# Kernel tuning notes

Measured on AMD Instinct MI355X. Metric: run time of the kernel, lower is better.

The kernel has to match this reference:

```python
import jax, jax.numpy as jnp
import numpy as np
import math

H = 8          # num_heads
HD = 64        # head_dim = hidden_dim // num_heads
LN_EPS = 1e-5


def setup_inputs() -> dict:
    key = jax.random.key(0)
    ks = jax.random.split(key, 16)
    B, N, L, D = 16, 1024, 7, 512
    s = 1.0 / math.sqrt(D)
    current_features = jax.random.normal(ks[0], (B, N, D), jnp.float32)
    lagged_features = jax.random.normal(ks[1], (B, N, L, D), jnp.float32)
    lag_weights = jnp.ones((L,), jnp.float32)
    Wq = jax.random.normal(ks[2], (D, D), jnp.float32) * s
    bq = jnp.zeros((D,), jnp.float32)
    Wk = jax.random.normal(ks[3], (D, D), jnp.float32) * s
    bk = jnp.zeros((D,), jnp.float32)
    Wv = jax.random.normal(ks[4], (D, D), jnp.float32) * s
    bv = jnp.zeros((D,), jnp.float32)
    Wo = jax.random.normal(ks[5], (D, D), jnp.float32) * s
    bo = jnp.zeros((D,), jnp.float32)
    adj = jax.random.uniform(ks[6], (N, N), jnp.float32)
    adj_prior = adj / (jnp.sum(adj, axis=-1, keepdims=True) + 1e-8)
    ln_g = jnp.ones((D,), jnp.float32)
    ln_b = jnp.zeros((D,), jnp.float32)
    return dict(current_features=current_features, lagged_features=lagged_features,
                lag_weights=lag_weights, Wq=Wq, bq=bq, Wk=Wk, bk=bk, Wv=Wv, bv=bv,
                Wo=Wo, bo=bo, adj_prior=adj_prior, ln_g=ln_g, ln_b=ln_b)


def _layer_norm(x, g, b):
    mu = jnp.mean(x, axis=-1, keepdims=True)
    var = jnp.mean(jnp.square(x - mu), axis=-1, keepdims=True)
    return (x - mu) * jax.lax.rsqrt(var + LN_EPS) * g + b


def reference(current_features, lagged_features, lag_weights, Wq, bq, Wk, bk,
              Wv, bv, Wo, bo, adj_prior, ln_g, ln_b):
    B, N, D = current_features.shape
    # lag-weighted aggregation of past states
    lag_w = jax.nn.softmax(lag_weights)
    lagged_agg = jnp.einsum('bnld,l->bnd', lagged_features, lag_w)
    # projections (torch Linear: x @ W.T + b)
    Q = current_features @ Wq.T + bq
    K = lagged_agg @ Wk.T + bk
    V = lagged_agg @ Wv.T + bv
    Q = Q.reshape(B, N, H, HD)
    K = K.reshape(B, N, H, HD)
    V = V.reshape(B, N, H, HD)
    scale = math.sqrt(HD)
    # scores [B, H, N, N] with additive adjacency bias
    scores = jnp.einsum('bnhd,bmhd->bhnm', Q, K) / scale
    scores = scores + adj_prior[None, None, :, :] * 0.5
    attn = jax.nn.softmax(scores, axis=-1)
    out = jnp.einsum('bhnm,bmhd->bnhd', attn, V).reshape(B, N, D)
    out = out @ Wo.T + bo
    return _layer_norm(current_features + out, ln_g, ln_b)
```

## Files before the change

### kernel.cpp

```cpp
#include <hip/hip_runtime.h>
#include <math.h>

#define B_  16
#define N_  1024
#define L_  7
#define D_  512
#define H_  8
#define HD_ 64
#define BN_ (B_ * N_)

typedef __attribute__((ext_vector_type(4))) float f32x4;
typedef __attribute__((ext_vector_type(8))) short bf16x8;

__device__ __forceinline__ unsigned short f2bf(float f) {
  unsigned int u = __float_as_uint(f);
  u += 0x7fffu + ((u >> 16) & 1u);
  return (unsigned short)(u >> 16);
}
__device__ __forceinline__ unsigned int pack2(float lo, float hi) {
  return (unsigned int)f2bf(lo) | ((unsigned int)f2bf(hi) << 16);
}
__device__ __forceinline__ void load_lds16(const unsigned short* g, unsigned short* s) {
  __builtin_amdgcn_global_load_lds(
      (const __attribute__((address_space(1))) void*)g,
      (__attribute__((address_space(3))) void*)s, 16, 0, 0);
}

__global__ __launch_bounds__(256)
void cast_bf16_kernel(const float* __restrict__ src, unsigned short* __restrict__ dst,
                      int n8) {
  const int i = blockIdx.x * 256 + threadIdx.x;
  if (i >= n8) return;
  const float4 a = ((const float4*)src)[2 * i];
  const float4 b = ((const float4*)src)[2 * i + 1];
  uint4 o;
  o.x = pack2(a.x, a.y); o.y = pack2(a.z, a.w);
  o.z = pack2(b.x, b.y); o.w = pack2(b.z, b.w);
  ((uint4*)dst)[i] = o;
}

__global__ __launch_bounds__(256)
void lag_agg_bf16_kernel(const float* __restrict__ lf, const float* __restrict__ lw,
                         unsigned short* __restrict__ out) {
  const int i = blockIdx.x * 256 + threadIdx.x;
  float wv[L_];
  float m = -INFINITY;
#pragma unroll
  for (int l = 0; l < L_; ++l) { wv[l] = lw[l]; m = fmaxf(m, wv[l]); }
  float s = 0.f;
#pragma unroll
  for (int l = 0; l < L_; ++l) { wv[l] = __expf(wv[l] - m); s += wv[l]; }
  const float inv = 1.f / s;

  const int d8 = i & (D_ / 8 - 1);
  const int bn = i >> 6;
  const float* src = lf + (size_t)bn * (L_ * D_) + d8 * 8;
  float acc[8] = {};
#pragma unroll
  for (int l = 0; l < L_; ++l) {
    const float4 v0 = *(const float4*)(src + l * D_);
    const float4 v1 = *(const float4*)(src + l * D_ + 4);
    const float wl = wv[l] * inv;
    acc[0] += v0.x * wl; acc[1] += v0.y * wl; acc[2] += v0.z * wl; acc[3] += v0.w * wl;
    acc[4] += v1.x * wl; acc[5] += v1.y * wl; acc[6] += v1.z * wl; acc[7] += v1.w * wl;
  }
  uint4 o;
  o.x = pack2(acc[0], acc[1]); o.y = pack2(acc[2], acc[3]);
  o.z = pack2(acc[4], acc[5]); o.w = pack2(acc[6], acc[7]);
  ((uint4*)out)[i] = o;
}

template<int MODE>
__global__ __launch_bounds__(256)
void gemm_bf16_kernel(const unsigned short* __restrict__ A,
                      const unsigned short* __restrict__ W,
                      const float* __restrict__ bias,
                      void* __restrict__ Cout) {
  __shared__ unsigned short As[128 * 64];
  __shared__ unsigned short Bs[128 * 64];
  const int t = threadIdx.x;
  const int w = t >> 6, l = t & 63;
  const int wm = w >> 1, wn = w & 1;
  const int lc = l & 15, lg = l >> 4;
  const int m0 = blockIdx.y << 7, n0 = blockIdx.x << 7;
  const int srow = l >> 3, sc = l & 7;

  f32x4 acc[4][4];
#pragma unroll
  for (int i = 0; i < 4; ++i)
#pragma unroll
    for (int j = 0; j < 4; ++j)
#pragma unroll
      for (int e = 0; e < 4; ++e) acc[i][j][e] = 0.f;

  for (int k0 = 0; k0 < D_; k0 += 64) {
    __syncthreads();
#pragma unroll
    for (int i = 0; i < 4; ++i) {
      const int rb = (w << 5) + (i << 3);
      const int row = rb + srow;
      const int c = sc ^ (row & 7);
      load_lds16(A + (size_t)(m0 + row) * D_ + k0 + (c << 3), As + rb * 64);
      load_lds16(W + (size_t)(n0 + row) * D_ + k0 + (c << 3), Bs + rb * 64);
    }
    __syncthreads();
#pragma unroll
    for (int kb = 0; kb < 2; ++kb) {
      bf16x8 af[4], bfr[4];
#pragma unroll
      for (int mi = 0; mi < 4; ++mi) {
        const int row = (wm << 6) + (mi << 4) + lc;
        const int pos = ((kb << 2) + lg) ^ (row & 7);
        af[mi] = *(const bf16x8*)(As + row * 64 + (pos << 3));
      }
#pragma unroll
      for (int ni = 0; ni < 4; ++ni) {
        const int row = (wn << 6) + (ni << 4) + lc;
        const int pos = ((kb << 2) + lg) ^ (row & 7);
        bfr[ni] = *(const bf16x8*)(Bs + row * 64 + (pos << 3));
      }
#pragma unroll
      for (int mi = 0; mi < 4; ++mi)
#pragma unroll
        for (int ni = 0; ni < 4; ++ni)
          acc[mi][ni] = __builtin_amdgcn_mfma_f32_16x16x32_bf16(
              af[mi], bfr[ni], acc[mi][ni], 0, 0, 0);
    }
  }
#pragma unroll
  for (int ni = 0; ni < 4; ++ni) {
    const int n = n0 + (wn << 6) + (ni << 4) + lc;
    const float bv = bias[n];
#pragma unroll
    for (int mi = 0; mi < 4; ++mi) {
      const int mb = m0 + (wm << 6) + (mi << 4) + (lg << 2);
      if (MODE == 2) {
        float* O = (float*)Cout;
#pragma unroll
        for (int e = 0; e < 4; ++e)
          O[(size_t)(mb + e) * D_ + n] = acc[mi][ni][e] + bv;
      } else if (MODE == 0) {
        unsigned short* O = (unsigned short*)Cout;
#pragma unroll
        for (int e = 0; e < 4; ++e)
          O[(size_t)(mb + e) * D_ + n] = f2bf(acc[mi][ni][e] + bv);
      } else {
        unsigned short* O = (unsigned short*)Cout;
        const int bb = mb >> 10, hh = n >> 6, d = n & 63;
        uint2 pk;
        pk.x = pack2(acc[mi][ni][0] + bv, acc[mi][ni][1] + bv);
        pk.y = pack2(acc[mi][ni][2] + bv, acc[mi][ni][3] + bv);
        *(uint2*)(O + ((size_t)((bb << 3) + hh) * HD_ + d) * N_ + (mb & 1023)) = pk;
      }
    }
  }
}

__global__ __launch_bounds__(256)
void attn_bf16_kernel(const unsigned short* __restrict__ Q,
                      const unsigned short* __restrict__ K,
                      const unsigned short* __restrict__ Vt,
                      const float* __restrict__ adj,
                      unsigned short* __restrict__ Out) {
  const int bh = blockIdx.y, b = bh >> 3, h = bh & 7;
  const int q0 = blockIdx.x << 6;
  const int t = threadIdx.x, w = t >> 6, l = t & 63;
  const int lc = l & 15, lg = l >> 4;
  __shared__ unsigned short Qs[64 * 64];
  __shared__ unsigned short Ks[64 * 64];
  __shared__ unsigned short Vs[64 * 64];
  const unsigned short* Qg = Q + (size_t)b * N_ * D_ + h * HD_;
  const unsigned short* Kg = K + (size_t)b * N_ * D_ + h * HD_;
  const unsigned short* Vg = Vt + (size_t)((b << 3) + h) * HD_ * N_;

#pragma unroll
  for (int i = 0; i < 2; ++i) {
    const int rb = (w << 4) + (i << 3);
    const int row = rb + (l >> 3);
    const int c = (l & 7) ^ (row & 7);
    load_lds16(Qg + (size_t)(q0 + row) * D_ + (c << 3), Qs + rb * 64);
  }

  float m_r = -INFINITY, l_r = 0.f;
  f32x4 o[4];
#pragma unroll
  for (int di = 0; di < 4; ++di)
#pragma unroll
    for (int e = 0; e < 4; ++e) o[di][e] = 0.f;
  const int myq = q0 + (w << 4) + lc;

  for (int kt = 0; kt < 16; ++kt) {
    const int kv0 = kt << 6;
#pragma unroll
    for (int i = 0; i < 2; ++i) {
      const int rb = (w << 4) + (i << 3);
      const int row = rb + (l >> 3);
      const int c = (l & 7) ^ (row & 7);
      load_lds16(Kg + (size_t)(kv0 + row) * D_ + (c << 3), Ks + rb * 64);
      load_lds16(Vg + (size_t)row * N_ + kv0 + (c << 3), Vs + rb * 64);
    }
    f32x4 aj[4];
#pragma unroll
    for (int ni = 0; ni < 4; ++ni)
      aj[ni] = *(const f32x4*)(adj + (size_t)myq * N_ + kv0 + (ni << 4) + (lg << 2));
    __syncthreads();

    bf16x8 qf[2];
#pragma unroll
    for (int kb = 0; kb < 2; ++kb) {
      const int row = (w << 4) + lc;
      const int pos = ((kb << 2) + lg) ^ (row & 7);
      qf[kb] = *(const bf16x8*)(Qs + row * 64 + (pos << 3));
    }
    f32x4 st[4];
#pragma unroll
    for (int ni = 0; ni < 4; ++ni)
#pragma unroll
      for (int e = 0; e < 4; ++e) st[ni][e] = 0.f;
#pragma unroll
    for (int ni = 0; ni < 4; ++ni)
#pragma unroll
      for (int kb = 0; kb < 2; ++kb) {
        const int row = (ni << 4) + lc;
        const int pos = ((kb << 2) + lg) ^ (row & 7);
        const bf16x8 kf = *(const bf16x8*)(Ks + row * 64 + (pos << 3));
        st[ni] = __builtin_amdgcn_mfma_f32_16x16x32_bf16(kf, qf[kb], st[ni], 0, 0, 0);
      }

    float tmax = -INFINITY;
#pragma unroll
    for (int ni = 0; ni < 4; ++ni)
#pragma unroll
      for (int e = 0; e < 4; ++e) {
        const float v = st[ni][e] * 0.125f + 0.5f * aj[ni][e];
        st[ni][e] = v;
        tmax = fmaxf(tmax, v);
      }
    tmax = fmaxf(tmax, __shfl_xor(tmax, 16));
    tmax = fmaxf(tmax, __shfl_xor(tmax, 32));
    const float mnew = fmaxf(m_r, tmax);
    const float alpha = __expf(m_r - mnew);
    float ts = 0.f;
#pragma unroll
    for (int ni = 0; ni < 4; ++ni)
#pragma unroll
      for (int e = 0; e < 4; ++e) {
        const float p = __expf(st[ni][e] - mnew);
        st[ni][e] = p;
        ts += p;
      }
    ts += __shfl_xor(ts, 16);
    ts += __shfl_xor(ts, 32);
    l_r = l_r * alpha + ts;
    m_r = mnew;
#pragma unroll
    for (int di = 0; di < 4; ++di)
#pragma unroll
      for (int e = 0; e < 4; ++e) o[di][e] *= alpha;

    unsigned int p2[4][2];
#pragma unroll
    for (int ni = 0; ni < 4; ++ni) {
      p2[ni][0] = pack2(st[ni][0], st[ni][1]);
      p2[ni][1] = pack2(st[ni][2], st[ni][3]);
    }
    const int sA = lc + ((lg & 1) << 5);
    const int sB = sA + 16;
    const bool hiq = lg >= 2;
#pragma unroll
    for (int kb = 0; kb < 2; ++kb) {
      const unsigned int dA0 = (unsigned int)__shfl((int)p2[2 * kb][0], sA);
      const unsigned int dA1 = (unsigned int)__shfl((int)p2[2 * kb][1], sA);
      const unsigned int dA2 = (unsigned int)__shfl((int)p2[2 * kb][0], sB);
      const unsigned int dA3 = (unsigned int)__shfl((int)p2[2 * kb][1], sB);
      const unsigned int dB0 = (unsigned int)__shfl((int)p2[2 * kb + 1][0], sA);
      const unsigned int dB1 = (unsigned int)__shfl((int)p2[2 * kb + 1][1], sA);
      const unsigned int dB2 = (unsigned int)__shfl((int)p2[2 * kb + 1][0], sB);
      const unsigned int dB3 = (unsigned int)__shfl((int)p2[2 * kb + 1][1], sB);
      union { unsigned int u[4]; bf16x8 v; } pb;
      pb.u[0] = hiq ? dB0 : dA0;
      pb.u[1] = hiq ? dB1 : dA1;
      pb.u[2] = hiq ? dB2 : dA2;
      pb.u[3] = hiq ? dB3 : dA3;
#pragma unroll
      for (int di = 0; di < 4; ++di) {
        const int row = (di << 4) + lc;
        const int pos = ((kb << 2) + lg) ^ (row & 7);
        const bf16x8 vf = *(const bf16x8*)(Vs + row * 64 + (pos << 3));
        o[di] = __builtin_amdgcn_mfma_f32_16x16x32_bf16(vf, pb.v, o[di], 0, 0, 0);
      }
    }
    __syncthreads();
  }
  const float inv = 1.f / l_r;
  unsigned short* Ob = Out + (size_t)(b * N_ + q0 + (w << 4) + lc) * D_ + h * HD_;
#pragma unroll
  for (int di = 0; di < 4; ++di) {
    uint2 pk;
    pk.x = pack2(o[di][0] * inv, o[di][1] * inv);
    pk.y = pack2(o[di][2] * inv, o[di][3] * inv);
    *(uint2*)(Ob + (di << 4) + (lg << 2)) = pk;
  }
}

__global__ __launch_bounds__(256)
void ln_kernel(float* __restrict__ Y, const float* __restrict__ Xr,
               const float* __restrict__ g, const float* __restrict__ bta) {
  const int row  = (blockIdx.x << 2) + (threadIdx.x >> 6);
  const int lane = threadIdx.x & 63;
  float* yrow = Y + (size_t)row * D_;
  const float* xrow = Xr + (size_t)row * D_;
  const int c0 = lane << 3;

  const float4 y0 = *(const float4*)(yrow + c0);
  const float4 y1 = *(const float4*)(yrow + c0 + 4);
  const float4 r0 = *(const float4*)(xrow + c0);
  const float4 r1 = *(const float4*)(xrow + c0 + 4);
  float x[8] = {y0.x + r0.x, y0.y + r0.y, y0.z + r0.z, y0.w + r0.w,
                y1.x + r1.x, y1.y + r1.y, y1.z + r1.z, y1.w + r1.w};

  float sum = 0.f;
#pragma unroll
  for (int u = 0; u < 8; ++u) sum += x[u];
#pragma unroll
  for (int off = 32; off >= 1; off >>= 1) sum += __shfl_xor(sum, off);
  const float mu = sum * (1.f / D_);

  float vs = 0.f;
#pragma unroll
  for (int u = 0; u < 8; ++u) { const float d = x[u] - mu; vs += d * d; }
#pragma unroll
  for (int off = 32; off >= 1; off >>= 1) vs += __shfl_xor(vs, off);
  const float var = vs * (1.f / D_) + 1e-5f;
  float rinv = rsqrtf(var);
  rinv = rinv * (1.5f - 0.5f * var * rinv * rinv);

  const float4 g0 = *(const float4*)(g + c0);
  const float4 g1 = *(const float4*)(g + c0 + 4);
  const float4 b0 = *(const float4*)(bta + c0);
  const float4 b1 = *(const float4*)(bta + c0 + 4);
  float4 o0, o1;
  o0.x = (x[0] - mu) * rinv * g0.x + b0.x;
  o0.y = (x[1] - mu) * rinv * g0.y + b0.y;
  o0.z = (x[2] - mu) * rinv * g0.z + b0.z;
  o0.w = (x[3] - mu) * rinv * g0.w + b0.w;
  o1.x = (x[4] - mu) * rinv * g1.x + b1.x;
  o1.y = (x[5] - mu) * rinv * g1.y + b1.y;
  o1.z = (x[6] - mu) * rinv * g1.z + b1.z;
  o1.w = (x[7] - mu) * rinv * g1.w + b1.w;
  *(float4*)(yrow + c0) = o0;
  *(float4*)(yrow + c0 + 4) = o1;
}

extern "C" void kernel_launch(void* const* d_in, const int* in_sizes, int n_in,
                              void* d_out, int out_size, void* d_ws, size_t ws_size,
                              hipStream_t stream) {
  const float* cur = (const float*)d_in[0];
  const float* lf  = (const float*)d_in[1];
  const float* lw  = (const float*)d_in[2];
  const float* Wq  = (const float*)d_in[3];
  const float* bq  = (const float*)d_in[4];
  const float* Wk  = (const float*)d_in[5];
  const float* bk  = (const float*)d_in[6];
  const float* Wv  = (const float*)d_in[7];
  const float* bv  = (const float*)d_in[8];
  const float* Wo  = (const float*)d_in[9];
  const float* bo  = (const float*)d_in[10];
  const float* adj = (const float*)d_in[11];
  const float* lng = (const float*)d_in[12];
  const float* lnb = (const float*)d_in[13];
  float* out = (float*)d_out;

  const size_t NE = (size_t)BN_ * D_;
  unsigned short* wsb   = (unsigned short*)d_ws;
  unsigned short* curb  = wsb;
  unsigned short* laggb = wsb + NE;
  unsigned short* Qb    = wsb + 2 * NE;
  unsigned short* Kb    = wsb + 3 * NE;
  unsigned short* Vtb   = wsb + 4 * NE;
  unsigned short* attnb = wsb + 5 * NE;
  unsigned short* Wqb   = wsb + 6 * NE;
  unsigned short* Wkb   = Wqb + (size_t)D_ * D_;
  unsigned short* Wvb   = Wkb + (size_t)D_ * D_;
  unsigned short* Wob   = Wvb + (size_t)D_ * D_;

  cast_bf16_kernel<<<BN_ * D_ / 8 / 256, 256, 0, stream>>>(cur, curb, BN_ * D_ / 8);
  cast_bf16_kernel<<<D_ * D_ / 8 / 256, 256, 0, stream>>>(Wq, Wqb, D_ * D_ / 8);
  cast_bf16_kernel<<<D_ * D_ / 8 / 256, 256, 0, stream>>>(Wk, Wkb, D_ * D_ / 8);
  cast_bf16_kernel<<<D_ * D_ / 8 / 256, 256, 0, stream>>>(Wv, Wvb, D_ * D_ / 8);
  cast_bf16_kernel<<<D_ * D_ / 8 / 256, 256, 0, stream>>>(Wo, Wob, D_ * D_ / 8);
  lag_agg_bf16_kernel<<<BN_ * D_ / 8 / 256, 256, 0, stream>>>(lf, lw, laggb);

  const dim3 gg(D_ / 128, BN_ / 128);
  gemm_bf16_kernel<0><<<gg, 256, 0, stream>>>(curb,  Wqb, bq, (void*)Qb);
  gemm_bf16_kernel<0><<<gg, 256, 0, stream>>>(laggb, Wkb, bk, (void*)Kb);
  gemm_bf16_kernel<1><<<gg, 256, 0, stream>>>(laggb, Wvb, bv, (void*)Vtb);
  attn_bf16_kernel<<<dim3(N_ / 64, B_ * H_), 256, 0, stream>>>(Qb, Kb, Vtb, adj, attnb);
  gemm_bf16_kernel<2><<<gg, 256, 0, stream>>>(attnb, Wob, bo, (void*)out);
  ln_kernel<<<BN_ / 4, 256, 0, stream>>>(out, cur, lng, lnb);
}
```

Measured before the change: 573.4 us.

## Double-buffer GEMM and attention tiles, batch QKV GEMMs and weight casts

The GEMM and attention kernels now use double-buffered LDS, prefetching the next K/V or A/W tile while the current one is computed. This removes one barrier per iteration and hides global-load latency. The three QKV projection GEMMs go out as one grid with a job selector, and the four weight casts are merged into one kernel, cutting launch count. Attention reuses the Q shared buffer, after Q fragments are hoisted to registers, to re-layout P through LDS instead of cross-lane shuffles; this doubles LDS per block, which may lower occupancy.

```diff
diff --git a/kernel.cpp b/kernel.cpp
--- a/kernel.cpp
+++ b/kernel.cpp
@@ -40,6 +40,23 @@
 }
 
 __global__ __launch_bounds__(256)
+void cast_w4_kernel(const float* __restrict__ w0, const float* __restrict__ w1,
+                    const float* __restrict__ w2, const float* __restrict__ w3,
+                    unsigned short* __restrict__ o0, unsigned short* __restrict__ o1,
+                    unsigned short* __restrict__ o2, unsigned short* __restrict__ o3) {
+  const int y = blockIdx.y;
+  const float* src = (y == 0) ? w0 : (y == 1) ? w1 : (y == 2) ? w2 : w3;
+  unsigned short* dst = (y == 0) ? o0 : (y == 1) ? o1 : (y == 2) ? o2 : o3;
+  const int i = blockIdx.x * 256 + threadIdx.x;
+  const float4 a = ((const float4*)src)[2 * i];
+  const float4 b = ((const float4*)src)[2 * i + 1];
+  uint4 o;
+  o.x = pack2(a.x, a.y); o.y = pack2(a.z, a.w);
+  o.z = pack2(b.x, b.y); o.w = pack2(b.z, b.w);
+  ((uint4*)dst)[i] = o;
+}
+
+__global__ __launch_bounds__(256)
 void lag_agg_bf16_kernel(const float* __restrict__ lf, const float* __restrict__ lw,
                          unsigned short* __restrict__ out) {
   const int i = blockIdx.x * 256 + threadIdx.x;
@@ -70,40 +87,62 @@
   ((uint4*)out)[i] = o;
 }
 
-template<int MODE>
-__global__ __launch_bounds__(256)
-void gemm_bf16_kernel(const unsigned short* __restrict__ A,
-                      const unsigned short* __restrict__ W,
-                      const float* __restrict__ bias,
-                      void* __restrict__ Cout) {
-  __shared__ unsigned short As[128 * 64];
-  __shared__ unsigned short Bs[128 * 64];
+struct GJob {
+  const unsigned short* A;
+  const unsigned short* W;
+  const float* bias;
+  void* C;
+  int mode;
+};
+
+__global__ __launch_bounds__(256)
+void gemm_dbuf_kernel(GJob j0, GJob j1, GJob j2) {
+  const GJob j = (blockIdx.z == 0) ? j0 : (blockIdx.z == 1) ? j1 : j2;
+  __shared__ unsigned short As[2 * 128 * 64];
+  __shared__ unsigned short Bs[2 * 128 * 64];
   const int t = threadIdx.x;
   const int w = t >> 6, l = t & 63;
   const int wm = w >> 1, wn = w & 1;
   const int lc = l & 15, lg = l >> 4;
   const int m0 = blockIdx.y << 7, n0 = blockIdx.x << 7;
   const int srow = l >> 3, sc = l & 7;
+  const unsigned short* A = j.A;
+  const unsigned short* W = j.W;
 
   f32x4 acc[4][4];
 #pragma unroll
   for (int i = 0; i < 4; ++i)
 #pragma unroll
-    for (int j = 0; j < 4; ++j)
-#pragma unroll
-      for (int e = 0; e < 4; ++e) acc[i][j][e] = 0.f;
-
+    for (int jj = 0; jj < 4; ++jj)
+#pragma unroll
+      for (int e = 0; e < 4; ++e) acc[i][jj][e] = 0.f;
+
+#pragma unroll
+  for (int i = 0; i < 4; ++i) {
+    const int rb = (w << 5) + (i << 3);
+    const int row = rb + srow;
+    const int c = sc ^ (row & 7);
+    load_lds16(A + (size_t)(m0 + row) * D_ + (c << 3), As + rb * 64);
+    load_lds16(W + (size_t)(n0 + row) * D_ + (c << 3), Bs + rb * 64);
+  }
+
+  int cur = 0;
   for (int k0 = 0; k0 < D_; k0 += 64) {
     __syncthreads();
-#pragma unroll
-    for (int i = 0; i < 4; ++i) {
-      const int rb = (w << 5) + (i << 3);
-      const int row = rb + srow;
-      const int c = sc ^ (row & 7);
-      load_lds16(A + (size_t)(m0 + row) * D_ + k0 + (c << 3), As + rb * 64);
-      load_lds16(W + (size_t)(n0 + row) * D_ + k0 + (c << 3), Bs + rb * 64);
-    }
-    __syncthreads();
+    if (k0 + 64 < D_) {
+      unsigned short* An = As + ((cur ^ 1) << 13);
+      unsigned short* Bn = Bs + ((cur ^ 1) << 13);
+#pragma unroll
+      for (int i = 0; i < 4; ++i) {
+        const int rb = (w << 5) + (i << 3);
+        const int row = rb + srow;
+        const int c = sc ^ (row & 7);
+        load_lds16(A + (size_t)(m0 + row) * D_ + k0 + 64 + (c << 3), An + rb * 64);
+        load_lds16(W + (size_t)(n0 + row) * D_ + k0 + 64 + (c << 3), Bn + rb * 64);
+      }
+    }
+    const unsigned short* Ac = As + (cur << 13);
+    const unsigned short* Bc = Bs + (cur << 13);
 #pragma unroll
     for (int kb = 0; kb < 2; ++kb) {
       bf16x8 af[4], bfr[4];
@@ -111,13 +150,13 @@
       for (int mi = 0; mi < 4; ++mi) {
         const int row = (wm << 6) + (mi << 4) + lc;
         const int pos = ((kb << 2) + lg) ^ (row & 7);
-        af[mi] = *(const bf16x8*)(As + row * 64 + (pos << 3));
+        af[mi] = *(const bf16x8*)(Ac + row * 64 + (pos << 3));
       }
 #pragma unroll
       for (int ni = 0; ni < 4; ++ni) {
         const int row = (wn << 6) + (ni << 4) + lc;
         const int pos = ((kb << 2) + lg) ^ (row & 7);
-        bfr[ni] = *(const bf16x8*)(Bs + row * 64 + (pos << 3));
+        bfr[ni] = *(const bf16x8*)(Bc + row * 64 + (pos << 3));
       }
 #pragma unroll
       for (int mi = 0; mi < 4; ++mi)
@@ -126,26 +165,29 @@
           acc[mi][ni] = __builtin_amdgcn_mfma_f32_16x16x32_bf16(
               af[mi], bfr[ni], acc[mi][ni], 0, 0, 0);
     }
-  }
+    cur ^= 1;
+  }
+
+  const int mode = j.mode;
 #pragma unroll
   for (int ni = 0; ni < 4; ++ni) {
     const int n = n0 + (wn << 6) + (ni << 4) + lc;
-    const float bv = bias[n];
+    const float bv = j.bias[n];
 #pragma unroll
     for (int mi = 0; mi < 4; ++mi) {
       const int mb = m0 + (wm << 6) + (mi << 4) + (lg << 2);
-      if (MODE == 2) {
-        float* O = (float*)Cout;
+      if (mode == 2) {
+        float* O = (float*)j.C;
 #pragma unroll
         for (int e = 0; e < 4; ++e)
           O[(size_t)(mb + e) * D_ + n] = acc[mi][ni][e] + bv;
-      } else if (MODE == 0) {
-        unsigned short* O = (unsigned short*)Cout;
+      } else if (mode == 0) {
+        unsigned short* O = (unsigned short*)j.C;
 #pragma unroll
         for (int e = 0; e < 4; ++e)
           O[(size_t)(mb + e) * D_ + n] = f2bf(acc[mi][ni][e] + bv);
       } else {
-        unsigned short* O = (unsigned short*)Cout;
+        unsigned short* O = (unsigned short*)j.C;
         const int bb = mb >> 10, hh = n >> 6, d = n & 63;
         uint2 pk;
         pk.x = pack2(acc[mi][ni][0] + bv, acc[mi][ni][1] + bv);
@@ -167,8 +209,8 @@
   const int t = threadIdx.x, w = t >> 6, l = t & 63;
   const int lc = l & 15, lg = l >> 4;
   __shared__ unsigned short Qs[64 * 64];
-  __shared__ unsigned short Ks[64 * 64];
-  __shared__ unsigned short Vs[64 * 64];
+  __shared__ unsigned short Ks[2 * 64 * 64];
+  __shared__ unsigned short Vs[2 * 64 * 64];
   const unsigned short* Qg = Q + (size_t)b * N_ * D_ + h * HD_;
   const unsigned short* Kg = K + (size_t)b * N_ * D_ + h * HD_;
   const unsigned short* Vg = Vt + (size_t)((b << 3) + h) * HD_ * N_;
@@ -179,6 +221,17 @@
     const int row = rb + (l >> 3);
     const int c = (l & 7) ^ (row & 7);
     load_lds16(Qg + (size_t)(q0 + row) * D_ + (c << 3), Qs + rb * 64);
+    load_lds16(Kg + (size_t)row * D_ + (c << 3), Ks + rb * 64);
+    load_lds16(Vg + (size_t)row * N_ + (c << 3), Vs + rb * 64);
+  }
+  __syncthreads();
+
+  bf16x8 qf[2];
+#pragma unroll
+  for (int kb = 0; kb < 2; ++kb) {
+    const int row = (w << 4) + lc;
+    const int pos = ((kb << 2) + lg) ^ (row & 7);
+    qf[kb] = *(const bf16x8*)(Qs + row * 64 + (pos << 3));
   }
 
   float m_r = -INFINITY, l_r = 0.f;
@@ -188,30 +241,32 @@
 #pragma unroll
     for (int e = 0; e < 4; ++e) o[di][e] = 0.f;
   const int myq = q0 + (w << 4) + lc;
-
+  unsigned short* Pw = Qs + (w << 10);
+
+  int cur = 0;
   for (int kt = 0; kt < 16; ++kt) {
+    if (kt) __syncthreads();
     const int kv0 = kt << 6;
-#pragma unroll
-    for (int i = 0; i < 2; ++i) {
-      const int rb = (w << 4) + (i << 3);
-      const int row = rb + (l >> 3);
-      const int c = (l & 7) ^ (row & 7);
-      load_lds16(Kg + (size_t)(kv0 + row) * D_ + (c << 3), Ks + rb * 64);
-      load_lds16(Vg + (size_t)row * N_ + kv0 + (c << 3), Vs + rb * 64);
+    if (kt < 15) {
+      unsigned short* Kn = Ks + ((cur ^ 1) << 12);
+      unsigned short* Vn = Vs + ((cur ^ 1) << 12);
+#pragma unroll
+      for (int i = 0; i < 2; ++i) {
+        const int rb = (w << 4) + (i << 3);
+        const int row = rb + (l >> 3);
+        const int c = (l & 7) ^ (row & 7);
+        load_lds16(Kg + (size_t)(kv0 + 64 + row) * D_ + (c << 3), Kn + rb * 64);
+        load_lds16(Vg + (size_t)row * N_ + kv0 + 64 + (c << 3), Vn + rb * 64);
+      }
     }
     f32x4 aj[4];
 #pragma unroll
     for (int ni = 0; ni < 4; ++ni)
       aj[ni] = *(const f32x4*)(adj + (size_t)myq * N_ + kv0 + (ni << 4) + (lg << 2));
-    __syncthreads();
-
-    bf16x8 qf[2];
-#pragma unroll
-    for (int kb = 0; kb < 2; ++kb) {
-      const int row = (w << 4) + lc;
-      const int pos = ((kb << 2) + lg) ^ (row & 7);
-      qf[kb] = *(const bf16x8*)(Qs + row * 64 + (pos << 3));
-    }
+
+    const unsigned short* Kc = Ks + (cur << 12);
+    const unsigned short* Vc = Vs + (cur << 12);
+
     f32x4 st[4];
 #pragma unroll
     for (int ni = 0; ni < 4; ++ni)
@@ -223,7 +278,7 @@
       for (int kb = 0; kb < 2; ++kb) {
         const int row = (ni << 4) + lc;
         const int pos = ((kb << 2) + lg) ^ (row & 7);
-        const bf16x8 kf = *(const bf16x8*)(Ks + row * 64 + (pos << 3));
+        const bf16x8 kf = *(const bf16x8*)(Kc + row * 64 + (pos << 3));
         st[ni] = __builtin_amdgcn_mfma_f32_16x16x32_bf16(kf, qf[kb], st[ni], 0, 0, 0);
       }
 
@@ -258,40 +313,30 @@
 #pragma unroll
       for (int e = 0; e < 4; ++e) o[di][e] *= alpha;
 
-    unsigned int p2[4][2];
 #pragma unroll
     for (int ni = 0; ni < 4; ++ni) {
-      p2[ni][0] = pack2(st[ni][0], st[ni][1]);
-      p2[ni][1] = pack2(st[ni][2], st[ni][3]);
-    }
-    const int sA = lc + ((lg & 1) << 5);
-    const int sB = sA + 16;
-    const bool hiq = lg >= 2;
+      uint2 pr;
+      pr.x = pack2(st[ni][0], st[ni][1]);
+      pr.y = pack2(st[ni][2], st[ni][3]);
+      const int schunk = (2 * ni + (lg >> 1)) ^ (lc & 7);
+      *(uint2*)(Pw + lc * 64 + (schunk << 3) + ((lg & 1) << 2)) = pr;
+    }
+
 #pragma unroll
     for (int kb = 0; kb < 2; ++kb) {
-      const unsigned int dA0 = (unsigned int)__shfl((int)p2[2 * kb][0], sA);
-      const unsigned int dA1 = (unsigned int)__shfl((int)p2[2 * kb][1], sA);
-      const unsigned int dA2 = (unsigned int)__shfl((int)p2[2 * kb][0], sB);
-      const unsigned int dA3 = (unsigned int)__shfl((int)p2[2 * kb][1], sB);
-      const unsigned int dB0 = (unsigned int)__shfl((int)p2[2 * kb + 1][0], sA);
-      const unsigned int dB1 = (unsigned int)__shfl((int)p2[2 * kb + 1][1], sA);
-      const unsigned int dB2 = (unsigned int)__shfl((int)p2[2 * kb + 1][0], sB);
-      const unsigned int dB3 = (unsigned int)__shfl((int)p2[2 * kb + 1][1], sB);
-      union { unsigned int u[4]; bf16x8 v; } pb;
-      pb.u[0] = hiq ? dB0 : dA0;
-      pb.u[1] = hiq ? dB1 : dA1;
-      pb.u[2] = hiq ? dB2 : dA2;
-      pb.u[3] = hiq ? dB3 : dA3;
+      const int rchunk = ((kb << 2) + lg) ^ (lc & 7);
+      const bf16x8 pb = *(const bf16x8*)(Pw + lc * 64 + (rchunk << 3));
 #pragma unroll
       for (int di = 0; di < 4; ++di) {
         const int row = (di << 4) + lc;
         const int pos = ((kb << 2) + lg) ^ (row & 7);
-        const bf16x8 vf = *(const bf16x8*)(Vs + row * 64 + (pos << 3));
-        o[di] = __builtin_amdgcn_mfma_f32_16x16x32_bf16(vf, pb.v, o[di], 0, 0, 0);
-      }
-    }
-    __syncthreads();
-  }
+        const bf16x8 vf = *(const bf16x8*)(Vc + row * 64 + (pos << 3));
+        o[di] = __builtin_amdgcn_mfma_f32_16x16x32_bf16(vf, pb, o[di], 0, 0, 0);
+      }
+    }
+    cur ^= 1;
+  }
+
   const float inv = 1.f / l_r;
   unsigned short* Ob = Out + (size_t)(b * N_ + q0 + (w << 4) + lc) * D_ + h * HD_;
 #pragma unroll
@@ -385,17 +430,19 @@
   unsigned short* Wob   = Wvb + (size_t)D_ * D_;
 
   cast_bf16_kernel<<<BN_ * D_ / 8 / 256, 256, 0, stream>>>(cur, curb, BN_ * D_ / 8);
-  cast_bf16_kernel<<<D_ * D_ / 8 / 256, 256, 0, stream>>>(Wq, Wqb, D_ * D_ / 8);
-  cast_bf16_kernel<<<D_ * D_ / 8 / 256, 256, 0, stream>>>(Wk, Wkb, D_ * D_ / 8);
-  cast_bf16_kernel<<<D_ * D_ / 8 / 256, 256, 0, stream>>>(Wv, Wvb, D_ * D_ / 8);
-  cast_bf16_kernel<<<D_ * D_ / 8 / 256, 256, 0, stream>>>(Wo, Wob, D_ * D_ / 8);
+  cast_w4_kernel<<<dim3(D_ * D_ / 8 / 256, 4), 256, 0, stream>>>(
+      Wq, Wk, Wv, Wo, Wqb, Wkb, Wvb, Wob);
   lag_agg_bf16_kernel<<<BN_ * D_ / 8 / 256, 256, 0, stream>>>(lf, lw, laggb);
 
-  const dim3 gg(D_ / 128, BN_ / 128);
-  gemm_bf16_kernel<0><<<gg, 256, 0, stream>>>(curb,  Wqb, bq, (void*)Qb);
-  gemm_bf16_kernel<0><<<gg, 256, 0, stream>>>(laggb, Wkb, bk, (void*)Kb);
-  gemm_bf16_kernel<1><<<gg, 256, 0, stream>>>(laggb, Wvb, bv, (void*)Vtb);
+  GJob jq{curb,  Wqb, bq, (void*)Qb,  0};
+  GJob jk{laggb, Wkb, bk, (void*)Kb,  0};
+  GJob jv{laggb, Wvb, bv, (void*)Vtb, 1};
+  gemm_dbuf_kernel<<<dim3(D_ / 128, BN_ / 128, 3), 256, 0, stream>>>(jq, jk, jv);
+
   attn_bf16_kernel<<<dim3(N_ / 64, B_ * H_), 256, 0, stream>>>(Qb, Kb, Vtb, adj, attnb);
-  gemm_bf16_kernel<2><<<gg, 256, 0, stream>>>(attnb, Wob, bo, (void*)out);
+
+  GJob jo{attnb, Wob, bo, (void*)out, 2};
+  gemm_dbuf_kernel<<<dim3(D_ / 128, BN_ / 128, 1), 256, 0, stream>>>(jo, jo, jo);
+
   ln_kernel<<<BN_ / 4, 256, 0, stream>>>(out, cur, lng, lnb);
 }
```

Result: no change. 583.9 us (+1.8%).
